# Performance work log

Hardware: AMD Instinct MI355X
Metric: run time of the kernel (lower is better)

## Reference

```python
import jax, jax.numpy as jnp
import numpy as np

N_ATOMS = 65536
N_BONDS = 98304
N_MOLS = 4096
D_IN = 128
D = 256  # d_e = d_v = d_u
REPEAT = 3


def setup_inputs() -> dict:
    key = jax.random.key(0)
    ks = jax.random.split(key, 12)
    atoms = jax.random.normal(ks[0], (N_ATOMS, D_IN), dtype=jnp.float32)
    bond_orders = jax.random.uniform(ks[1], (N_BONDS,), dtype=jnp.float32)
    bond_src = jax.random.randint(ks[2], (N_BONDS,), 0, N_ATOMS, dtype=jnp.int32)
    bond_dst = jax.random.randint(ks[3], (N_BONDS,), 0, N_ATOMS, dtype=jnp.int32)
    atom_mol = jnp.sort(jax.random.randint(ks[4], (N_ATOMS,), 0, N_MOLS, dtype=jnp.int32))
    bond_mol = jnp.sort(jax.random.randint(ks[5], (N_BONDS,), 0, N_MOLS, dtype=jnp.int32))
    def w(k, fan_in, fan_out):
        return jax.random.normal(k, (fan_in, fan_out), dtype=jnp.float32) / np.sqrt(fan_in)
    W_fe = w(ks[6], 1, D)
    W_fv = w(ks[7], D_IN, D)
    W_fu = w(ks[8], D_IN, D)
    W_e = w(ks[9], 5 * D, D)   # [h_e, h_e0, h_left, h_right, u_e]
    W_v = w(ks[10], 4 * D, D)  # [h_v, h_v0, e_bar_v, u_v]
    W_u = w(ks[11], 4 * D, D)  # [h_u, h_u0, e_bar, v_bar]
    return {"atoms": atoms, "bond_orders": bond_orders, "bond_src": bond_src,
            "bond_dst": bond_dst, "atom_mol": atom_mol, "bond_mol": bond_mol,
            "W_fe": W_fe, "W_fv": W_fv, "W_fu": W_fu,
            "W_e": W_e, "W_v": W_v, "W_u": W_u}


def _graphnet(atoms, bond_orders, bond_src, bond_dst, atom_mol, bond_mol,
              W_fe, W_fv, W_fu, W_e, W_v, W_u):
    seg_sum = lambda x, ids: jax.ops.segment_sum(x, ids, num_segments=N_MOLS)
    # f_e / f_v: initial edge / node embeddings
    h_e0 = jnp.tanh(bond_orders[:, None] @ W_fe)          # [n_bonds, D]
    h_v0 = jnp.tanh(atoms @ W_fv)                          # [n_atoms, D]
    # f_u: per-molecule mean of raw atom features -> global embedding
    counts = seg_sum(jnp.ones((atoms.shape[0], 1), atoms.dtype), atom_mol)
    mol_mean = seg_sum(atoms, atom_mol) / jnp.maximum(counts, 1.0)
    h_u0 = jnp.tanh(mol_mean @ W_fu)                       # [n_mols, D]

    def step(carry, _):
        h_e, h_v, h_u = carry
        # pairwise_update is identity (default) -> per-mol loop is a no-op
        h_left = h_v[bond_src]                             # gather endpoints
        h_right = h_v[bond_dst]
        u_e = h_u[bond_mol]                                # global attr per edge
        h_e = jnp.tanh(jnp.concatenate([h_e, h_e0, h_left, h_right, u_e], axis=1) @ W_e)
        # rho_e_v: sum edge updates into both endpoint atoms
        e_bar_v = jnp.zeros_like(h_v).at[bond_src].add(h_e).at[bond_dst].add(h_e)
        u_v = h_u[atom_mol]                                # global attr per atom
        h_v = jnp.tanh(jnp.concatenate([h_v, h_v0, e_bar_v, u_v], axis=1) @ W_v)
        # rho_e_u / rho_v_u: per-molecule segment sums
        e_bar = seg_sum(h_e, bond_mol)
        v_bar = seg_sum(h_v, atom_mol)
        h_u = jnp.tanh(jnp.concatenate([h_u, h_u0, e_bar, v_bar], axis=1) @ W_u)
        return (h_e, h_v, h_u), None

    (h_e, h_v, h_u), _ = jax.lax.scan(step, (h_e0, h_v0, h_u0), None, length=REPEAT)
    # f_r default returns its first argument: the final edge representation
    return h_e


def reference(atoms, bond_orders, bond_src, bond_dst, atom_mol, bond_mol,
              W_fe, W_fv, W_fu, W_e, W_v, W_u):
    return _graphnet(atoms, bond_orders, bond_src, bond_dst, atom_mol, bond_mol,
                     W_fe, W_fv, W_fu, W_e, W_v, W_u)
```

## Files before the change

kernel.cpp:

```cpp
#include <hip/hip_runtime.h>
#include <cstdint>
#include <cmath>

#define N_ATOMS 65536
#define N_BONDS 98304
#define N_MOLS  4096
#define D_IN    128
#define DD      256
#define REPEAT  3

typedef __attribute__((ext_vector_type(8))) short short8;
typedef __attribute__((ext_vector_type(4))) float f32x4;
typedef unsigned short ushort_t;

__device__ __forceinline__ unsigned short f2h(float f) {
  union { _Float16 h; unsigned short u; } x; x.h = (_Float16)f; return x.u;
}
__device__ __forceinline__ float h2f(unsigned short u) {
  union { unsigned short u; _Float16 h; } x; x.u = u; return (float)x.h;
}

#define GLD16(gp, lp) __builtin_amdgcn_global_load_lds( \
    (const __attribute__((address_space(1))) void*)(gp), \
    (__attribute__((address_space(3))) void*)(lp), 16, 0, 0)

template<int NSEG, int SEGW, int BM>
__global__ __launch_bounds__(BM * 4)
void mfma_concat_gemm(const ushort_t* __restrict__ s0, const int* __restrict__ i0,
                      const ushort_t* __restrict__ s1, const int* __restrict__ i1,
                      const ushort_t* __restrict__ s2, const int* __restrict__ i2,
                      const ushort_t* __restrict__ s3, const int* __restrict__ i3,
                      const ushort_t* __restrict__ s4, const int* __restrict__ i4,
                      const ushort_t* __restrict__ Wt,
                      ushort_t* __restrict__ ob, ushort_t* __restrict__ ob2,
                      float* __restrict__ of)
{
  constexpr int NT     = BM * 4;
  constexpr int KW     = NSEG * SEGW;
  constexpr int SPS    = SEGW / 32;
  constexpr int ABYTES = BM * 64;
  constexpr int BI     = 16384 / (NT * 16);

  __shared__ __align__(16) char smem[ABYTES + 16384];

  const int t      = threadIdx.x;
  const int m0     = blockIdx.x * BM;
  const int srcoff = (((t & 3) ^ ((t >> 2) & 3) ^ ((t >> 4) & 3)) << 4);
  const int toff   = t * 16;

  uint32_t aoff[5];
  {
    const int rg = m0 + (t >> 2);
    const int* ips[5] = { i0, i1, i2, i3, i4 };
    #pragma unroll
    for (int s = 0; s < NSEG; ++s) {
      int idx = ips[s] ? ips[s][rg] : rg;
      aoff[s] = (uint32_t)idx * (SEGW * 2);
    }
  }

  const char* wtb[4];
  #pragma unroll
  for (int i = 0; i < BI; ++i)
    wtb[i] = (const char*)Wt + (size_t)((i * (NT >> 2) + (t >> 2)) * KW) * 2 + srcoff;

  f32x4 acc[4][4];
  const f32x4 z = {0.f, 0.f, 0.f, 0.f};
  #pragma unroll
  for (int a = 0; a < 4; ++a)
    #pragma unroll
    for (int b = 0; b < 4; ++b) acc[a][b] = z;

  const int l   = t & 63;
  const int wid = t >> 6;
  const int wr  = wid >> 2;
  const int wc  = wid & 3;
  const int swz = (((l >> 4) ^ (l & 3) ^ ((l >> 2) & 3)) << 4);
  const int aro = wr * 4096 + (l & 15) * 64 + swz;
  const int bro = ABYTES + wc * 4096 + (l & 15) * 64 + swz;

  int kt = 0;
  #pragma unroll
  for (int seg = 0; seg < NSEG; ++seg) {
    const ushort_t* sp = seg == 0 ? s0 : seg == 1 ? s1 : seg == 2 ? s2 : seg == 3 ? s3 : s4;
    const char* arow = (const char*)sp + aoff[seg];
    for (int sub = 0; sub < SPS; ++sub, ++kt) {
      GLD16(arow + sub * 64 + srcoff, smem + toff);
      #pragma unroll
      for (int i = 0; i < BI; ++i)
        GLD16(wtb[i] + (size_t)kt * 64, smem + ABYTES + i * (NT * 16) + toff);
      __syncthreads();

      short8 af[4], bfv[4];
      #pragma unroll
      for (int mf = 0; mf < 4; ++mf) af[mf]  = *(const short8*)(smem + aro + mf * 1024);
      #pragma unroll
      for (int nf = 0; nf < 4; ++nf) bfv[nf] = *(const short8*)(smem + bro + nf * 1024);
      #pragma unroll
      for (int mf = 0; mf < 4; ++mf)
        #pragma unroll
        for (int nf = 0; nf < 4; ++nf)
          acc[mf][nf] = __builtin_amdgcn_mfma_f32_16x16x32_f16(af[mf], bfv[nf], acc[mf][nf], 0, 0, 0);
      __syncthreads();
    }
  }

  const int colb = wc * 64 + (l & 15);
  const int rowb = m0 + wr * 64 + ((l >> 4) << 2);
  #pragma unroll
  for (int mf = 0; mf < 4; ++mf) {
    #pragma unroll
    for (int nf = 0; nf < 4; ++nf) {
      f32x4 d = acc[mf][nf];
      #pragma unroll
      for (int r = 0; r < 4; ++r) {
        float v = tanhf(d[r]);
        size_t o = (size_t)(rowb + mf * 16 + r) * DD + colb + nf * 16;
        unsigned short hv16 = f2h(v);
        ob[o] = hv16;
        if (ob2) ob2[o] = hv16;
        if (of)  of[o]  = v;
      }
    }
  }
}


__global__ __launch_bounds__(256)
void f32_to_f16(const float* __restrict__ in, ushort_t* __restrict__ out, int n4) {
  int t = blockIdx.x * 256 + threadIdx.x;
  if (t >= n4) return;
  float4 v = ((const float4*)in)[t];
  ushort4 o; o.x = f2h(v.x); o.y = f2h(v.y); o.z = f2h(v.z); o.w = f2h(v.w);
  ((ushort4*)out)[t] = o;
}

__global__ __launch_bounds__(256)
void transpose_w(const float* __restrict__ in, ushort_t* __restrict__ out, int K) {
  int t = blockIdx.x * 256 + threadIdx.x;
  int n = t / K, k = t - n * K;
  out[t] = f2h(in[(size_t)k * DD + n]);
}

__global__ __launch_bounds__(256)
void init_he0_k(const float* __restrict__ bo, const float* __restrict__ wfe,
                ushort_t* __restrict__ he0, ushort_t* __restrict__ he) {
  int t = blockIdx.x * 256 + threadIdx.x;
  int b = t >> 6, c = (t & 63) << 2;
  float o = bo[b];
  float4 w = *(const float4*)&wfe[c];
  ushort4 v;
  v.x = f2h(tanhf(o * w.x)); v.y = f2h(tanhf(o * w.y));
  v.z = f2h(tanhf(o * w.z)); v.w = f2h(tanhf(o * w.w));
  size_t idx = ((size_t)b * DD + c) >> 2;
  ((ushort4*)he0)[idx] = v; ((ushort4*)he)[idx] = v;
}

__global__ __launch_bounds__(256)
void mol_accum(const float* __restrict__ atoms, const int* __restrict__ amol,
               float* __restrict__ msum, float* __restrict__ cnt) {
  int t = blockIdx.x * 256 + threadIdx.x;
  int a = t >> 5, c = (t & 31) << 2;
  float4 v = *(const float4*)&atoms[(size_t)a * D_IN + c];
  int m = amol[a];
  float* p = &msum[(size_t)m * D_IN + c];
  unsafeAtomicAdd(p + 0, v.x); unsafeAtomicAdd(p + 1, v.y);
  unsafeAtomicAdd(p + 2, v.z); unsafeAtomicAdd(p + 3, v.w);
  if ((t & 31) == 0) unsafeAtomicAdd(&cnt[m], 1.0f);
}

__global__ __launch_bounds__(256)
void mol_mean_h(const float* __restrict__ msum, const float* __restrict__ cnt,
                ushort_t* __restrict__ mmean) {
  int t = blockIdx.x * 256 + threadIdx.x;
  int m = t >> 5, c = (t & 31) << 2;
  float inv = 1.0f / fmaxf(cnt[m], 1.0f);
  float4 v = *(const float4*)&msum[(size_t)m * D_IN + c];
  ushort4 o; o.x = f2h(v.x * inv); o.y = f2h(v.y * inv);
  o.z = f2h(v.z * inv); o.w = f2h(v.w * inv);
  ((ushort4*)mmean)[((size_t)m * D_IN + c) >> 2] = o;
}


__global__ __launch_bounds__(256)
void count_deg(const int* __restrict__ src, const int* __restrict__ dst,
               int* __restrict__ deg) {
  int b = blockIdx.x * 256 + threadIdx.x;
  if (b >= N_BONDS) return;
  atomicAdd(&deg[src[b]], 1);
  atomicAdd(&deg[dst[b]], 1);
}

__global__ __launch_bounds__(256)
void scan_deg(const int* __restrict__ deg, int* __restrict__ rowptr,
              int* __restrict__ cursor) {
  __shared__ int partial[256];
  int t = threadIdx.x;
  int base = t * 256;
  int s = 0;
  for (int i = 0; i < 256; ++i) s += deg[base + i];
  partial[t] = s;
  __syncthreads();
  if (t == 0) {
    int acc = 0;
    for (int i = 0; i < 256; ++i) { int v = partial[i]; partial[i] = acc; acc += v; }
    rowptr[N_ATOMS] = acc;
  }
  __syncthreads();
  int acc = partial[t];
  for (int i = 0; i < 256; ++i) {
    rowptr[base + i] = acc; cursor[base + i] = acc;
    acc += deg[base + i];
  }
}

__global__ __launch_bounds__(256)
void fill_csr(const int* __restrict__ src, const int* __restrict__ dst,
              int* __restrict__ cursor, int* __restrict__ list) {
  int b = blockIdx.x * 256 + threadIdx.x;
  if (b >= N_BONDS) return;
  int p = atomicAdd(&cursor[src[b]], 1); list[p] = b;
  int q = atomicAdd(&cursor[dst[b]], 1); list[q] = b;
}

__global__ __launch_bounds__(256)
void gather_ebv(const ushort_t* __restrict__ he, const int* __restrict__ rowptr,
                const int* __restrict__ list, ushort_t* __restrict__ ebv_h) {
  int t = blockIdx.x * 256 + threadIdx.x;
  int a = t >> 6, c = (t & 63) << 2;
  int s = rowptr[a], e = rowptr[a + 1];
  float a0 = 0.f, a1 = 0.f, a2 = 0.f, a3 = 0.f;
  for (int i = s; i < e; ++i) {
    int b = list[i];
    ushort4 v = *(const ushort4*)&he[(size_t)b * DD + c];
    a0 += h2f(v.x); a1 += h2f(v.y); a2 += h2f(v.z); a3 += h2f(v.w);
  }
  ushort4 o; o.x = f2h(a0); o.y = f2h(a1); o.z = f2h(a2); o.w = f2h(a3);
  ((ushort4*)ebv_h)[((size_t)a * DD + c) >> 2] = o;
}

__global__ __launch_bounds__(256)
void seg_sum_sorted(const ushort_t* __restrict__ x, const int* __restrict__ ids,
                    float* __restrict__ out) {
  __shared__ int sid[64];
  int r0 = blockIdx.x * 64;
  int c  = threadIdx.x;
  if (c < 64) sid[c] = ids[r0 + c];
  __syncthreads();
  float acc = 0.f; int prev = sid[0];
  const ushort_t* p = x + (size_t)r0 * DD + c;
  for (int r = 0; r < 64; ++r, p += DD) {
    int id = sid[r];
    if (id != prev) { unsafeAtomicAdd(&out[(size_t)prev * DD + c], acc); acc = 0.f; prev = id; }
    acc += h2f(*p);
  }
  unsafeAtomicAdd(&out[(size_t)prev * DD + c], acc);
}


extern "C" void kernel_launch(void* const* d_in, const int* in_sizes, int n_in,
                              void* d_out, int out_size, void* d_ws, size_t ws_size,
                              hipStream_t stream)
{
  const float* atoms       = (const float*)d_in[0];
  const float* bond_orders = (const float*)d_in[1];
  const int*   bond_src    = (const int*)d_in[2];
  const int*   bond_dst    = (const int*)d_in[3];
  const int*   atom_mol    = (const int*)d_in[4];
  const int*   bond_mol    = (const int*)d_in[5];
  const float* W_fe        = (const float*)d_in[6];
  const float* W_fv        = (const float*)d_in[7];
  const float* W_fu        = (const float*)d_in[8];
  const float* W_e         = (const float*)d_in[9];
  const float* W_v         = (const float*)d_in[10];
  const float* W_u         = (const float*)d_in[11];

  char* w = (char*)d_ws;
  auto alloc = [&](size_t bytes) { char* p = w; w += (bytes + 255) & ~(size_t)255; return p; };

  ushort_t* atoms_h  = (ushort_t*)alloc((size_t)N_ATOMS * D_IN * 2);
  ushort_t* he0  = (ushort_t*)alloc((size_t)N_BONDS * DD * 2);
  ushort_t* he   = (ushort_t*)alloc((size_t)N_BONDS * DD * 2);
  ushort_t* hv0  = (ushort_t*)alloc((size_t)N_ATOMS * DD * 2);
  ushort_t* hv   = (ushort_t*)alloc((size_t)N_ATOMS * DD * 2);
  ushort_t* hu0  = (ushort_t*)alloc((size_t)N_MOLS * DD * 2);
  ushort_t* hu   = (ushort_t*)alloc((size_t)N_MOLS * DD * 2);
  ushort_t* mmean= (ushort_t*)alloc((size_t)N_MOLS * D_IN * 2);
  ushort_t* Wte  = (ushort_t*)alloc((size_t)DD * 1280 * 2);
  ushort_t* Wtv  = (ushort_t*)alloc((size_t)DD * 1024 * 2);
  ushort_t* Wtu  = (ushort_t*)alloc((size_t)DD * 1024 * 2);
  ushort_t* Wtfv = (ushort_t*)alloc((size_t)DD * D_IN * 2);
  ushort_t* Wtfu = (ushort_t*)alloc((size_t)DD * D_IN * 2);
  float* eb_f  = (float*)alloc((size_t)N_MOLS * DD * 4);
  float* vb_f  = (float*)alloc((size_t)N_MOLS * DD * 4);
  ushort_t* ebv_h = (ushort_t*)alloc((size_t)N_ATOMS * DD * 2);
  ushort_t* eb_h  = (ushort_t*)alloc((size_t)N_MOLS * DD * 2);
  ushort_t* vb_h  = (ushort_t*)alloc((size_t)N_MOLS * DD * 2);
  float* msum = (float*)alloc((size_t)N_MOLS * D_IN * 4);
  float* cnt  = (float*)alloc((size_t)N_MOLS * 4);
  int* deg    = (int*)alloc((size_t)N_ATOMS * 4);
  int* rowptr = (int*)alloc((size_t)(N_ATOMS + 1) * 4);
  int* cursor = (int*)alloc((size_t)N_ATOMS * 4);
  int* list   = (int*)alloc((size_t)2 * N_BONDS * 4);
  if ((size_t)(w - (char*)d_ws) > ws_size) return;

  const ushort_t* NU = nullptr; const int* NI = nullptr;

  f32_to_f16<<<N_ATOMS * D_IN / 4 / 256, 256, 0, stream>>>(atoms, atoms_h, N_ATOMS * D_IN / 4);
  transpose_w<<<DD * 1280 / 256, 256, 0, stream>>>(W_e, Wte, 1280);
  transpose_w<<<DD * 1024 / 256, 256, 0, stream>>>(W_v, Wtv, 1024);
  transpose_w<<<DD * 1024 / 256, 256, 0, stream>>>(W_u, Wtu, 1024);
  transpose_w<<<DD * D_IN / 256, 256, 0, stream>>>(W_fv, Wtfv, D_IN);
  transpose_w<<<DD * D_IN / 256, 256, 0, stream>>>(W_fu, Wtfu, D_IN);
  hipMemsetAsync(deg, 0, (size_t)N_ATOMS * 4, stream);
  count_deg<<<(N_BONDS + 255) / 256, 256, 0, stream>>>(bond_src, bond_dst, deg);
  scan_deg<<<1, 256, 0, stream>>>(deg, rowptr, cursor);
  fill_csr<<<(N_BONDS + 255) / 256, 256, 0, stream>>>(bond_src, bond_dst, cursor, list);

  hipMemsetAsync(msum, 0, (size_t)N_MOLS * D_IN * 4 + 4096 + N_MOLS * 4, stream);
  mol_accum<<<N_ATOMS * 32 / 256, 256, 0, stream>>>(atoms, atom_mol, msum, cnt);
  mol_mean_h<<<N_MOLS * 32 / 256, 256, 0, stream>>>(msum, cnt, mmean);
  init_he0_k<<<N_BONDS * 64 / 256, 256, 0, stream>>>(bond_orders, W_fe, he0, he);
  mfma_concat_gemm<1, 128, 128><<<N_ATOMS / 128, 512, 0, stream>>>(
      atoms_h, NI, NU, NI, NU, NI, NU, NI, NU, NI, Wtfv, hv0, hv, nullptr);
  mfma_concat_gemm<1, 128, 64><<<N_MOLS / 64, 256, 0, stream>>>(
      mmean, NI, NU, NI, NU, NI, NU, NI, NU, NI, Wtfu, hu0, hu, nullptr);

  for (int it = 0; it < REPEAT; ++it) {
    hipMemsetAsync(eb_f, 0, (size_t)2 * N_MOLS * DD * 4, stream);
    mfma_concat_gemm<5, 256, 128><<<N_BONDS / 128, 512, 0, stream>>>(
        he, NI, he0, NI, hv, bond_src, hv, bond_dst, hu, bond_mol,
        Wte, he, nullptr, it == REPEAT - 1 ? (float*)d_out : nullptr);
    gather_ebv<<<N_ATOMS * 64 / 256, 256, 0, stream>>>(he, rowptr, list, ebv_h);
    seg_sum_sorted<<<N_BONDS / 64, 256, 0, stream>>>(he, bond_mol, eb_f);
    mfma_concat_gemm<4, 256, 128><<<N_ATOMS / 128, 512, 0, stream>>>(
        hv, NI, hv0, NI, ebv_h, NI, hu, atom_mol, NU, NI,
        Wtv, hv, nullptr, nullptr);
    seg_sum_sorted<<<N_ATOMS / 64, 256, 0, stream>>>(hv, atom_mol, vb_f);
    f32_to_f16<<<2 * N_MOLS * DD / 4 / 256, 256, 0, stream>>>(eb_f, eb_h, 2 * N_MOLS * DD / 4);
    mfma_concat_gemm<4, 256, 64><<<N_MOLS / 64, 256, 0, stream>>>(
        hu, NI, hu0, NI, eb_h, NI, vb_h, NI, NU, NI,
        Wtu, hu, nullptr, nullptr);
  }
}
```

Before: 1.243 ms.

## Double-buffer LDS tiles in concat GEMM and run-length reduce sorted molecule sums

The concat-gather GEMM now uses two shared-memory tile buffers and issues the async global-to-LDS loads for the next K tile before computing on the current one. This drops one barrier per step and overlaps load latency with MFMA work, at the cost of doubling LDS use, which may reduce blocks per CU. Separately, the per-molecule atom sum now relies on atom_mol being sorted. It accumulates runs of the same molecule in registers and emits one atomic per run instead of one per element.

```diff
diff --git a/kernel.cpp b/kernel.cpp
--- a/kernel.cpp
+++ b/kernel.cpp
@@ -39,23 +39,25 @@
   constexpr int KW     = NSEG * SEGW;
   constexpr int SPS    = SEGW / 32;
   constexpr int ABYTES = BM * 64;
+  constexpr int TILE   = ABYTES + 16384;
   constexpr int BI     = 16384 / (NT * 16);
 
-  __shared__ __align__(16) char smem[ABYTES + 16384];
+  __shared__ __align__(16) char smem[2 * TILE];
 
   const int t      = threadIdx.x;
   const int m0     = blockIdx.x * BM;
   const int srcoff = (((t & 3) ^ ((t >> 2) & 3) ^ ((t >> 4) & 3)) << 4);
   const int toff   = t * 16;
 
-  uint32_t aoff[5];
+  const char* arows[5];
   {
     const int rg = m0 + (t >> 2);
     const int* ips[5] = { i0, i1, i2, i3, i4 };
+    const ushort_t* sps[5] = { s0, s1, s2, s3, s4 };
     #pragma unroll
     for (int s = 0; s < NSEG; ++s) {
       int idx = ips[s] ? ips[s][rg] : rg;
-      aoff[s] = (uint32_t)idx * (SEGW * 2);
+      arows[s] = (const char*)sps[s] + (size_t)idx * (SEGW * 2);
     }
   }
 
@@ -79,29 +81,39 @@
   const int aro = wr * 4096 + (l & 15) * 64 + swz;
   const int bro = ABYTES + wc * 4096 + (l & 15) * 64 + swz;
 
-  int kt = 0;
+  auto stage_tile = [&](int segS, int sub, int db) {
+    GLD16(arows[segS] + sub * 64 + srcoff, smem + db + toff);
+    const int kt = segS * SPS + sub;
+    #pragma unroll
+    for (int i = 0; i < BI; ++i)
+      GLD16(wtb[i] + (size_t)kt * 64, smem + db + ABYTES + i * (NT * 16) + toff);
+  };
+  auto compute = [&](int sb) {
+    short8 af[4], bfv[4];
+    #pragma unroll
+    for (int mf = 0; mf < 4; ++mf) af[mf]  = *(const short8*)(smem + sb + aro + mf * 1024);
+    #pragma unroll
+    for (int nf = 0; nf < 4; ++nf) bfv[nf] = *(const short8*)(smem + sb + bro + nf * 1024);
+    #pragma unroll
+    for (int mf = 0; mf < 4; ++mf)
+      #pragma unroll
+      for (int nf = 0; nf < 4; ++nf)
+        acc[mf][nf] = __builtin_amdgcn_mfma_f32_16x16x32_f16(af[mf], bfv[nf], acc[mf][nf], 0, 0, 0);
+  };
+
+  stage_tile(0, 0, 0);
+  __syncthreads();
+
+  int cur = 0;
   #pragma unroll
   for (int seg = 0; seg < NSEG; ++seg) {
-    const ushort_t* sp = seg == 0 ? s0 : seg == 1 ? s1 : seg == 2 ? s2 : seg == 3 ? s3 : s4;
-    const char* arow = (const char*)sp + aoff[seg];
-    for (int sub = 0; sub < SPS; ++sub, ++kt) {
-      GLD16(arow + sub * 64 + srcoff, smem + toff);
-      #pragma unroll
-      for (int i = 0; i < BI; ++i)
-        GLD16(wtb[i] + (size_t)kt * 64, smem + ABYTES + i * (NT * 16) + toff);
+    for (int sub = 0; sub < SPS; ++sub) {
+      const int nb = (cur ^ 1) * TILE;
+      if (sub + 1 < SPS)            stage_tile(seg, sub + 1, nb);
+      else if (seg + 1 < NSEG)      stage_tile(seg + 1, 0, nb);
+      compute(cur * TILE);
       __syncthreads();
-
-      short8 af[4], bfv[4];
-      #pragma unroll
-      for (int mf = 0; mf < 4; ++mf) af[mf]  = *(const short8*)(smem + aro + mf * 1024);
-      #pragma unroll
-      for (int nf = 0; nf < 4; ++nf) bfv[nf] = *(const short8*)(smem + bro + nf * 1024);
-      #pragma unroll
-      for (int mf = 0; mf < 4; ++mf)
-        #pragma unroll
-        for (int nf = 0; nf < 4; ++nf)
-          acc[mf][nf] = __builtin_amdgcn_mfma_f32_16x16x32_f16(af[mf], bfv[nf], acc[mf][nf], 0, 0, 0);
-      __syncthreads();
+      cur ^= 1;
     }
   }
 
@@ -156,17 +168,27 @@
   ((ushort4*)he0)[idx] = v; ((ushort4*)he)[idx] = v;
 }
 
-__global__ __launch_bounds__(256)
-void mol_accum(const float* __restrict__ atoms, const int* __restrict__ amol,
-               float* __restrict__ msum, float* __restrict__ cnt) {
-  int t = blockIdx.x * 256 + threadIdx.x;
-  int a = t >> 5, c = (t & 31) << 2;
-  float4 v = *(const float4*)&atoms[(size_t)a * D_IN + c];
-  int m = amol[a];
-  float* p = &msum[(size_t)m * D_IN + c];
-  unsafeAtomicAdd(p + 0, v.x); unsafeAtomicAdd(p + 1, v.y);
-  unsafeAtomicAdd(p + 2, v.z); unsafeAtomicAdd(p + 3, v.w);
-  if ((t & 31) == 0) unsafeAtomicAdd(&cnt[m], 1.0f);
+__global__ __launch_bounds__(128)
+void mol_accum_sorted(const float* __restrict__ atoms, const int* __restrict__ amol,
+                      float* __restrict__ msum, float* __restrict__ cnt) {
+  __shared__ int sid[64];
+  int r0 = blockIdx.x * 64;
+  int c  = threadIdx.x;
+  if (c < 64) sid[c] = amol[r0 + c];
+  __syncthreads();
+  float acc = 0.f; int prev = sid[0]; int run = 0;
+  const float* p = atoms + (size_t)r0 * D_IN + c;
+  for (int r = 0; r < 64; ++r, p += D_IN) {
+    int id = sid[r];
+    if (id != prev) {
+      unsafeAtomicAdd(&msum[(size_t)prev * D_IN + c], acc);
+      if (c == 0) unsafeAtomicAdd(&cnt[prev], (float)run);
+      acc = 0.f; run = 0; prev = id;
+    }
+    acc += *p; run += 1;
+  }
+  unsafeAtomicAdd(&msum[(size_t)prev * D_IN + c], acc);
+  if (c == 0) unsafeAtomicAdd(&cnt[prev], (float)run);
 }
 
 __global__ __launch_bounds__(256)
@@ -317,8 +339,8 @@
   scan_deg<<<1, 256, 0, stream>>>(deg, rowptr, cursor);
   fill_csr<<<(N_BONDS + 255) / 256, 256, 0, stream>>>(bond_src, bond_dst, cursor, list);
 
-  hipMemsetAsync(msum, 0, (size_t)N_MOLS * D_IN * 4 + 4096 + N_MOLS * 4, stream);
-  mol_accum<<<N_ATOMS * 32 / 256, 256, 0, stream>>>(atoms, atom_mol, msum, cnt);
+  hipMemsetAsync(msum, 0, (size_t)(N_MOLS * D_IN + N_MOLS) * 4, stream);
+  mol_accum_sorted<<<N_ATOMS / 64, 128, 0, stream>>>(atoms, atom_mol, msum, cnt);
   mol_mean_h<<<N_MOLS * 32 / 256, 256, 0, stream>>>(msum, cnt, mmean);
   init_he0_k<<<N_BONDS * 64 / 256, 256, 0, stream>>>(bond_orders, W_fe, he0, he);
   mfma_concat_gemm<1, 128, 128><<<N_ATOMS / 128, 512, 0, stream>>>(
```

New measurement: 1.087 ms. 12.6% less time.
